# Kernel tuning notes

Measured on AMD Instinct MI355X. Metric: run time of the kernel, lower is better.

Reference implementation:

```python
import jax, jax.numpy as jnp
import numpy as np

B, S, E, H, K = 64, 512, 256, 512, 100


def setup_inputs() -> dict:
    key = jax.random.key(0)
    ks = jax.random.split(key, 7)
    scale = 0.02
    return {
        "event_types": jax.random.randint(ks[0], (B, S), 0, K),
        "time_deltas": jax.random.uniform(ks[1], (B, S), dtype=jnp.float32),
        "embedding": jax.random.normal(ks[2], (K, E), dtype=jnp.float32) * scale,
        "W": jax.random.normal(ks[3], (E + H, 5 * H), dtype=jnp.float32) * scale,
        "b": jnp.zeros((5 * H,), dtype=jnp.float32),
        "Wi": jax.random.normal(ks[4], (H, K), dtype=jnp.float32) * scale,
        "bi": jnp.zeros((K,), dtype=jnp.float32),
    }


def _ctlstm_scan(x_seq, dt_seq, W, b, hidden_dim):
    """x_seq: [B,S,E], dt_seq: [B,S]. Returns h_seq [B,S,H], decay_seq [B,S,H]."""
    bsz = x_seq.shape[0]
    h0 = jnp.zeros((bsz, hidden_dim), x_seq.dtype)
    c0 = jnp.zeros((bsz, hidden_dim), x_seq.dtype)

    def step(carry, inp):
        h, c = carry
        x_t, dt_t = inp  # [B,E], [B]
        z = jnp.concatenate([x_t, h], axis=-1) @ W + b  # [B,5H]
        i, f, o, g, d = jnp.split(z, 5, axis=-1)
        i = jax.nn.sigmoid(i)
        f = jax.nn.sigmoid(f)
        o = jax.nn.sigmoid(o)
        g = jnp.tanh(g)
        decay = jax.nn.softplus(d)  # decay rate >= 0
        c_new = f * c + i * g
        c_t = c_new * jnp.exp(-decay * dt_t[:, None])  # continuous-time decay
        h_t = o * jnp.tanh(c_t)
        return (h_t, c_t), (h_t, decay)

    # time-major for scan
    xs = (jnp.swapaxes(x_seq, 0, 1), jnp.swapaxes(dt_seq, 0, 1))
    _, (h_seq, decay_seq) = jax.lax.scan(step, (h0, c0), xs)
    return jnp.swapaxes(h_seq, 0, 1), jnp.swapaxes(decay_seq, 0, 1)


def reference(event_types, time_deltas, embedding, W, b, Wi, bi):
    x_seq = embedding[event_types]  # [B,S,E]
    hidden_state, decay_rate = _ctlstm_scan(x_seq, time_deltas, W, b, H)
    base_intensities = jax.nn.softplus(hidden_state @ Wi + bi)  # [B,S,K]
    return hidden_state, decay_rate, base_intensities
```

## Files before the change

### kernel.cpp

```cpp
#include <hip/hip_runtime.h>
#include <hip/hip_bf16.h>
#include <stdint.h>

#define BB 64
#define SS 512
#define EE 256
#define HH 512
#define NWG 32

typedef short s16x8 __attribute__((ext_vector_type(8)));
typedef float vf4 __attribute__((ext_vector_type(4)));

#define OFF_WBT   0UL
#define OFF_EMB   3932160UL
#define OFF_WIT   3983360UL
#define OFF_DTT   4098048UL
#define OFF_FLAGS 4229120UL
#define OFF_HBUF  4491264UL
#define OFF_ZXP   38045696UL

__device__ __forceinline__ int fidx(int t, int w, int v) {
  return (((t >> 4) * 128) + w * 4 + v) * 16 + (t & 15);
}

__device__ __forceinline__ unsigned short f2bf(float f) {
  unsigned u = __float_as_uint(f);
  u += 0x7fffu + ((u >> 16) & 1u);
  return (unsigned short)(u >> 16);
}
__device__ __forceinline__ float bf2f(unsigned short h) {
  return __uint_as_float(((unsigned)h) << 16);
}
__device__ __forceinline__ float sigmoidf_(float x) { return 1.f / (1.f + __expf(-x)); }
__device__ __forceinline__ float softplusf_(float x) {
  return fmaxf(x, 0.f) + log1pf(__expf(-fabsf(x)));
}
__device__ __forceinline__ float tanhf_(float x) {
  float e = __expf(2.f * x);
  return 1.f - 2.f / (e + 1.f);
}

__global__ void init_kernel(const float* __restrict__ W, const float* __restrict__ emb,
                            const float* __restrict__ Wi, const float* __restrict__ td,
                            unsigned short* __restrict__ WbT, unsigned short* __restrict__ embB,
                            unsigned short* __restrict__ WiT, float* __restrict__ dtT,
                            int* __restrict__ flags) {
  unsigned i = blockIdx.x * 256u + threadIdx.x;
  if (i < 1966080u) {
    unsigned c = i / 768u, k = i % 768u;
    WbT[i] = f2bf(W[(size_t)k * 2560u + c]);
    return;
  }
  i -= 1966080u;
  if (i < 25600u) { embB[i] = f2bf(emb[i]); return; }
  i -= 25600u;
  if (i < 57344u) {
    unsigned c = i / 512u, k = i % 512u;
    WiT[i] = f2bf(c < 100u ? Wi[(size_t)k * 100u + c] : 0.f);
    return;
  }
  i -= 57344u;
  if (i < 32768u) {
    unsigned t = i / 64u, b = i % 64u;
    dtT[i] = td[(size_t)b * 512u + t];
    return;
  }
  i -= 32768u;
  if (i < 65536u) { flags[i] = 0; return; }
}

__global__ __launch_bounds__(256, 2)
void zx_kernel(const int* __restrict__ evt, const unsigned short* __restrict__ embB,
               const unsigned short* __restrict__ WbT, const float* __restrict__ bias,
               unsigned short* __restrict__ zxp) {
  const int t = blockIdx.y;
  const int tid = threadIdx.x;
  const int v = tid >> 6, lane = tid & 63;
  const int m = lane & 15, quad = lane >> 4;
  const int cbase = blockIdx.x * 256 + v * 64;

  s16x8 Breg[8][4];
#pragma unroll
  for (int cf = 0; cf < 4; ++cf) {
    const unsigned short* bp = WbT + (size_t)(cbase + cf * 16 + m) * 768 + quad * 8;
#pragma unroll
    for (int ch = 0; ch < 8; ++ch) Breg[ch][cf] = *(const s16x8*)(bp + ch * 32);
  }
  int ev[4];
#pragma unroll
  for (int rt = 0; rt < 4; ++rt) ev[rt] = evt[(size_t)(rt * 16 + m) * 512 + t];

  vf4 acc[4][4];
#pragma unroll
  for (int cf = 0; cf < 4; ++cf) {
    float bbv = bias[cbase + cf * 16 + m];
#pragma unroll
    for (int rt = 0; rt < 4; ++rt) acc[rt][cf] = (vf4){bbv, bbv, bbv, bbv};
  }
#pragma unroll
  for (int ch = 0; ch < 8; ++ch) {
#pragma unroll
    for (int rt = 0; rt < 4; ++rt) {
      s16x8 a = *(const s16x8*)(embB + (size_t)ev[rt] * 256 + ch * 32 + quad * 8);
#pragma unroll
      for (int cf = 0; cf < 4; ++cf)
        acc[rt][cf] = __builtin_amdgcn_mfma_f32_16x16x32_bf16(a, Breg[ch][cf], acc[rt][cf], 0, 0, 0);
    }
  }
#pragma unroll
  for (int cf = 0; cf < 4; ++cf) {
    int col0 = cbase + cf * 16;
    int g = col0 >> 9;
    int w = (col0 & 511) >> 4;
#pragma unroll
    for (int rt = 0; rt < 4; ++rt) {
      unsigned h0 = f2bf(acc[rt][cf][0]);
      unsigned h1 = f2bf(acc[rt][cf][1]);
      unsigned h2 = f2bf(acc[rt][cf][2]);
      unsigned h3 = f2bf(acc[rt][cf][3]);
      uint2 val;
      val.x = h0 | (h1 << 16);
      val.y = h2 | (h3 << 16);
      ((uint2*)zxp)[((((size_t)t * 32 + w) * 4 + rt) * 5 + g) * 64 + lane] = val;
    }
  }
}

__global__ __launch_bounds__(256, 1)
void scan_kernel(const unsigned short* __restrict__ WbT,
                 const unsigned short* __restrict__ zxp,
                 const float* __restrict__ dtT,
                 unsigned short* __restrict__ hbuf,
                 int* __restrict__ flags,
                 float* __restrict__ out_h, float* __restrict__ out_d) {
  const int w = blockIdx.x;
  const int tid = threadIdx.x;
  const int v = tid >> 6, lane = tid & 63;
  const int m = lane & 15, quad = lane >> 4;
  const int rowb = v * 16;
  const int bb0 = rowb + quad * 4;
  const int col = w * 16 + m;

  s16x8 Breg[16][5];
#pragma unroll
  for (int g = 0; g < 5; ++g) {
    const unsigned short* bp = WbT + (size_t)(g * 512 + w * 16 + m) * 768 + 256 + quad * 8;
#pragma unroll
    for (int ch = 0; ch < 16; ++ch) Breg[ch][g] = *(const s16x8*)(bp + ch * 32);
  }

  vf4 cst = (vf4){0.f, 0.f, 0.f, 0.f};

  for (int t = 0; t < 512; ++t) {
    vf4 acc[5];
#pragma unroll
    for (int g = 0; g < 5; ++g) {
      uint2 zv = ((const uint2*)zxp)[((((size_t)t * 32 + w) * 4 + v) * 5 + g) * 64 + lane];
      acc[g][0] = bf2f((unsigned short)(zv.x & 0xffffu));
      acc[g][1] = bf2f((unsigned short)(zv.x >> 16));
      acc[g][2] = bf2f((unsigned short)(zv.y & 0xffffu));
      acc[g][3] = bf2f((unsigned short)(zv.y >> 16));
    }
    vf4 dt4 = *(const vf4*)(dtT + t * 64 + bb0);

    if (t > 0) {
      const int tp = t - 1;
      if (lane < 32) {
        const int* fp = flags + fidx(tp, lane, v);
        while (__hip_atomic_load(fp, __ATOMIC_RELAXED, __HIP_MEMORY_SCOPE_AGENT) == 0) {
          __builtin_amdgcn_s_sleep(1);
        }
      }
      __asm__ __volatile__("" ::: "memory");
      const unsigned short* hsrc =
          hbuf + (size_t)tp * (BB * HH) + (size_t)(rowb + m) * HH + quad * 8;
#pragma unroll
      for (int ch = 0; ch < 16; ++ch) {
        s16x8 a = *(const s16x8*)(hsrc + ch * 32);
#pragma unroll
        for (int g = 0; g < 5; ++g)
          acc[g] = __builtin_amdgcn_mfma_f32_16x16x32_bf16(a, Breg[ch][g], acc[g], 0, 0, 0);
      }
    }

    float hv[4], dv[4];
#pragma unroll
    for (int r = 0; r < 4; ++r) {
      float i_ = sigmoidf_(acc[0][r]);
      float f_ = sigmoidf_(acc[1][r]);
      float o_ = sigmoidf_(acc[2][r]);
      float g_ = tanhf_(acc[3][r]);
      float dec = softplusf_(acc[4][r]);
      float cn = f_ * cst[r] + i_ * g_;
      float ct = cn * __expf(-dec * dt4[r]);
      float h_ = o_ * tanhf_(ct);
      cst[r] = ct;
      hv[r] = h_; dv[r] = dec;
      __hip_atomic_store(hbuf + (size_t)t * (BB * HH) + (size_t)(bb0 + r) * HH + col,
                         f2bf(h_), __ATOMIC_RELAXED, __HIP_MEMORY_SCOPE_AGENT);
    }
    __asm__ __volatile__("" ::: "memory");
    __builtin_amdgcn_s_waitcnt(0);
    __asm__ __volatile__("" ::: "memory");
    if (lane == 0) {
      __hip_atomic_store(flags + fidx(t, w, v), 1, __ATOMIC_RELAXED,
                         __HIP_MEMORY_SCOPE_AGENT);
    }
#pragma unroll
    for (int r = 0; r < 4; ++r) {
      size_t oo = ((size_t)(bb0 + r) * SS + t) * HH + col;
      out_h[oo] = hv[r];
      out_d[oo] = dv[r];
    }
  }
}

__global__ __launch_bounds__(256, 2)
void inten_kernel(const unsigned short* __restrict__ hbuf,
                  const unsigned short* __restrict__ WiT,
                  const float* __restrict__ bi,
                  float* __restrict__ out_i) {
  const int b = blockIdx.y;
  const int t0 = blockIdx.x * 64;
  const int tid = threadIdx.x;
  const int v = tid >> 6, lane = tid & 63;
  const int m = lane & 15, quad = lane >> 4;
  const int trow = t0 + v * 16 + m;

  vf4 acc[7];
#pragma unroll
  for (int cf = 0; cf < 7; ++cf) {
    int c = cf * 16 + m;
    float bbv = (c < 100) ? bi[c] : 0.f;
    acc[cf] = (vf4){bbv, bbv, bbv, bbv};
  }
  const unsigned short* ha = hbuf + ((size_t)trow * 64 + b) * 512 + quad * 8;
#pragma unroll 4
  for (int ch = 0; ch < 16; ++ch) {
    s16x8 a = *(const s16x8*)(ha + ch * 32);
#pragma unroll
    for (int cf = 0; cf < 7; ++cf) {
      s16x8 bf = *(const s16x8*)(WiT + (size_t)(cf * 16 + m) * 512 + ch * 32 + quad * 8);
      acc[cf] = __builtin_amdgcn_mfma_f32_16x16x32_bf16(a, bf, acc[cf], 0, 0, 0);
    }
  }
#pragma unroll
  for (int cf = 0; cf < 7; ++cf) {
    int c = cf * 16 + m;
#pragma unroll
    for (int r = 0; r < 4; ++r) {
      int tt = t0 + v * 16 + quad * 4 + r;
      if (c < 100) out_i[((size_t)b * 512 + tt) * 100 + c] = softplusf_(acc[cf][r]);
    }
  }
}

extern "C" void kernel_launch(void* const* d_in, const int* in_sizes, int n_in,
                              void* d_out, int out_size, void* d_ws, size_t ws_size,
                              hipStream_t stream) {
  (void)in_sizes; (void)n_in; (void)out_size; (void)ws_size;
  const int*   evt  = (const int*)d_in[0];
  const float* td   = (const float*)d_in[1];
  const float* emb  = (const float*)d_in[2];
  const float* W    = (const float*)d_in[3];
  const float* bias = (const float*)d_in[4];
  const float* Wi   = (const float*)d_in[5];
  const float* bi   = (const float*)d_in[6];

  char* ws = (char*)d_ws;
  unsigned short* WbT  = (unsigned short*)(ws + OFF_WBT);
  unsigned short* embB = (unsigned short*)(ws + OFF_EMB);
  unsigned short* WiT  = (unsigned short*)(ws + OFF_WIT);
  float*          dtT  = (float*)(ws + OFF_DTT);
  int*            flags= (int*)(ws + OFF_FLAGS);
  unsigned short* hbuf = (unsigned short*)(ws + OFF_HBUF);
  unsigned short* zxp  = (unsigned short*)(ws + OFF_ZXP);

  float* out_h = (float*)d_out;
  float* out_d = out_h + (size_t)BB * SS * HH;
  float* out_i = out_d + (size_t)BB * SS * HH;

  init_kernel<<<8390, 256, 0, stream>>>(W, emb, Wi, td, WbT, embB, WiT, dtT, flags);
  zx_kernel<<<dim3(10, 512), 256, 0, stream>>>(evt, embB, WbT, bias, zxp);
  scan_kernel<<<NWG, 256, 0, stream>>>(WbT, zxp, dtT, hbuf, flags, out_h, out_d);
  inten_kernel<<<dim3(8, 64), 256, 0, stream>>>(hbuf, WiT, bi, out_i);
}
```

Before: 3.703 ms.

## Split scan into batch groups with XCC-local sync and independent recurrences

The recurrent scan now runs on 64 workgroups instead of 32. It is split into 8 independent batch groups of 8 rows, and each group spreads the hidden columns over 8 workgroups, so a group only waits on its own 8 producers rather than on every workgroup. The h buffer and the zx layout are reorganised per batch group. At startup the kernel reads which XCC each workgroup landed on; if a group sits entirely on one XCC it uses workgroup-scope atomics and volatile stores for lower-latency flag polling. The cost is that half of each MFMA's 16 rows are padding, and the flag and XCC co-location handshake adds complexity and risk.

Result: slower. 4.878 ms (+31.7%).

```diff
diff --git a/kernel.cpp b/kernel.cpp
--- a/kernel.cpp
+++ b/kernel.cpp
@@ -6,7 +6,6 @@
 #define SS 512
 #define EE 256
 #define HH 512
-#define NWG 32
 
 typedef short s16x8 __attribute__((ext_vector_type(8)));
 typedef float vf4 __attribute__((ext_vector_type(4)));
@@ -16,11 +15,12 @@
 #define OFF_WIT   3983360UL
 #define OFF_DTT   4098048UL
 #define OFF_FLAGS 4229120UL
-#define OFF_HBUF  4491264UL
-#define OFF_ZXP   38045696UL
-
-__device__ __forceinline__ int fidx(int t, int w, int v) {
-  return (((t >> 4) * 128) + w * 4 + v) * 16 + (t & 15);
+#define OFF_CTL   4753408UL
+#define OFF_HB    4753920UL
+#define OFF_ZXP   38308352UL
+
+__device__ __forceinline__ int fidx(int t, int g, int L) {
+  return (((t >> 4) * 256) + g * 32 + L) * 16 + (t & 15);
 }
 
 __device__ __forceinline__ unsigned short f2bf(float f) {
@@ -66,7 +66,7 @@
     return;
   }
   i -= 32768u;
-  if (i < 65536u) { flags[i] = 0; return; }
+  if (i < 131200u) { flags[i] = 0; return; }
 }
 
 __global__ __launch_bounds__(256, 2)
@@ -110,10 +110,13 @@
 #pragma unroll
   for (int cf = 0; cf < 4; ++cf) {
     int col0 = cbase + cf * 16;
-    int g = col0 >> 9;
-    int w = (col0 & 511) >> 4;
+    int gate = col0 >> 9;
+    int hcol = col0 & 511;
+    int rr_ = hcol >> 6;
+    int vv = (hcol >> 4) & 3;
 #pragma unroll
     for (int rt = 0; rt < 4; ++rt) {
+      int gg = rt * 2 + (quad >> 1);
       unsigned h0 = f2bf(acc[rt][cf][0]);
       unsigned h1 = f2bf(acc[rt][cf][1]);
       unsigned h2 = f2bf(acc[rt][cf][2]);
@@ -121,7 +124,8 @@
       uint2 val;
       val.x = h0 | (h1 << 16);
       val.y = h2 | (h3 << 16);
-      ((uint2*)zxp)[((((size_t)t * 32 + w) * 4 + rt) * 5 + g) * 64 + lane] = val;
+      ((uint2*)zxp)[(((((size_t)t * 8 + gg) * 8 + rr_) * 4 + vv) * 5 + gate) * 32
+                    + (quad & 1) * 16 + m] = val;
     }
   }
 }
@@ -130,93 +134,127 @@
 void scan_kernel(const unsigned short* __restrict__ WbT,
                  const unsigned short* __restrict__ zxp,
                  const float* __restrict__ dtT,
-                 unsigned short* __restrict__ hbuf,
-                 int* __restrict__ flags,
+                 unsigned short* __restrict__ hb,
+                 int* __restrict__ flags, int* __restrict__ ctl,
                  float* __restrict__ out_h, float* __restrict__ out_d) {
-  const int w = blockIdx.x;
+  const int wg = blockIdx.x;
+  const int g = wg & 7, r = wg >> 3;
   const int tid = threadIdx.x;
   const int v = tid >> 6, lane = tid & 63;
   const int m = lane & 15, quad = lane >> 4;
-  const int rowb = v * 16;
-  const int bb0 = rowb + quad * 4;
-  const int col = w * 16 + m;
+  const int qh = quad & 1;
+  const int c0 = r * 64 + v * 16;
+  const int col = c0 + m;
+
+  __shared__ int s_loc;
+  if (tid == 0) {
+    unsigned xcc = __builtin_amdgcn_s_getreg(63508) & 0xfu;
+    __hip_atomic_store(&ctl[wg], (int)(xcc + 1u), __ATOMIC_RELAXED, __HIP_MEMORY_SCOPE_AGENT);
+    __hip_atomic_fetch_add(&ctl[64], 1, __ATOMIC_RELEASE, __HIP_MEMORY_SCOPE_AGENT);
+    while (__hip_atomic_load(&ctl[64], __ATOMIC_ACQUIRE, __HIP_MEMORY_SCOPE_AGENT) < 64)
+      __builtin_amdgcn_s_sleep(1);
+    int x0 = __hip_atomic_load(&ctl[g], __ATOMIC_RELAXED, __HIP_MEMORY_SCOPE_AGENT);
+    int lc = (x0 != 0);
+    for (int j = 1; j < 8; ++j)
+      lc &= (__hip_atomic_load(&ctl[g + 8 * j], __ATOMIC_RELAXED, __HIP_MEMORY_SCOPE_AGENT) == x0);
+    s_loc = lc;
+  }
+  __syncthreads();
+  const bool loc = (s_loc != 0);
 
   s16x8 Breg[16][5];
 #pragma unroll
-  for (int g = 0; g < 5; ++g) {
-    const unsigned short* bp = WbT + (size_t)(g * 512 + w * 16 + m) * 768 + 256 + quad * 8;
-#pragma unroll
-    for (int ch = 0; ch < 16; ++ch) Breg[ch][g] = *(const s16x8*)(bp + ch * 32);
+  for (int g5 = 0; g5 < 5; ++g5) {
+    const unsigned short* bp = WbT + (size_t)(g5 * 512 + c0 + m) * 768 + 256 + quad * 8;
+#pragma unroll
+    for (int ch = 0; ch < 16; ++ch) Breg[ch][g5] = *(const s16x8*)(bp + ch * 32);
   }
 
   vf4 cst = (vf4){0.f, 0.f, 0.f, 0.f};
 
   for (int t = 0; t < 512; ++t) {
     vf4 acc[5];
-#pragma unroll
-    for (int g = 0; g < 5; ++g) {
-      uint2 zv = ((const uint2*)zxp)[((((size_t)t * 32 + w) * 4 + v) * 5 + g) * 64 + lane];
-      acc[g][0] = bf2f((unsigned short)(zv.x & 0xffffu));
-      acc[g][1] = bf2f((unsigned short)(zv.x >> 16));
-      acc[g][2] = bf2f((unsigned short)(zv.y & 0xffffu));
-      acc[g][3] = bf2f((unsigned short)(zv.y >> 16));
-    }
-    vf4 dt4 = *(const vf4*)(dtT + t * 64 + bb0);
+    if (lane < 32) {
+#pragma unroll
+      for (int g5 = 0; g5 < 5; ++g5) {
+        uint2 zv = ((const uint2*)zxp)[(((((size_t)t * 8 + g) * 8 + r) * 4 + v) * 5 + g5) * 32 + lane];
+        acc[g5][0] = bf2f((unsigned short)(zv.x & 0xffffu));
+        acc[g5][1] = bf2f((unsigned short)(zv.x >> 16));
+        acc[g5][2] = bf2f((unsigned short)(zv.y & 0xffffu));
+        acc[g5][3] = bf2f((unsigned short)(zv.y >> 16));
+      }
+    } else {
+#pragma unroll
+      for (int g5 = 0; g5 < 5; ++g5) acc[g5] = (vf4){0.f, 0.f, 0.f, 0.f};
+    }
+    vf4 dt4 = *(const vf4*)(dtT + t * 64 + g * 8 + qh * 4);
 
     if (t > 0) {
       const int tp = t - 1;
       if (lane < 32) {
-        const int* fp = flags + fidx(tp, lane, v);
-        while (__hip_atomic_load(fp, __ATOMIC_RELAXED, __HIP_MEMORY_SCOPE_AGENT) == 0) {
-          __builtin_amdgcn_s_sleep(1);
+        int* fp = flags + fidx(tp, g, lane);
+        if (loc) {
+          while ((__hip_atomic_fetch_add(fp, 0x10000, __ATOMIC_RELAXED,
+                                         __HIP_MEMORY_SCOPE_WORKGROUP) & 0xffff) == 0) {}
+        } else {
+          while (__hip_atomic_load(fp, __ATOMIC_RELAXED, __HIP_MEMORY_SCOPE_AGENT) == 0)
+            __builtin_amdgcn_s_sleep(1);
         }
       }
       __asm__ __volatile__("" ::: "memory");
-      const unsigned short* hsrc =
-          hbuf + (size_t)tp * (BB * HH) + (size_t)(rowb + m) * HH + quad * 8;
+      const unsigned short* hsrc = hb + (((size_t)g * 512 + tp) * 8 + (m & 7)) * 512 + quad * 8;
 #pragma unroll
       for (int ch = 0; ch < 16; ++ch) {
         s16x8 a = *(const s16x8*)(hsrc + ch * 32);
 #pragma unroll
-        for (int g = 0; g < 5; ++g)
-          acc[g] = __builtin_amdgcn_mfma_f32_16x16x32_bf16(a, Breg[ch][g], acc[g], 0, 0, 0);
+        for (int g5 = 0; g5 < 5; ++g5)
+          acc[g5] = __builtin_amdgcn_mfma_f32_16x16x32_bf16(a, Breg[ch][g5], acc[g5], 0, 0, 0);
       }
     }
 
     float hv[4], dv[4];
 #pragma unroll
-    for (int r = 0; r < 4; ++r) {
-      float i_ = sigmoidf_(acc[0][r]);
-      float f_ = sigmoidf_(acc[1][r]);
-      float o_ = sigmoidf_(acc[2][r]);
-      float g_ = tanhf_(acc[3][r]);
-      float dec = softplusf_(acc[4][r]);
-      float cn = f_ * cst[r] + i_ * g_;
-      float ct = cn * __expf(-dec * dt4[r]);
+    for (int rr = 0; rr < 4; ++rr) {
+      float i_ = sigmoidf_(acc[0][rr]);
+      float f_ = sigmoidf_(acc[1][rr]);
+      float o_ = sigmoidf_(acc[2][rr]);
+      float g_ = tanhf_(acc[3][rr]);
+      float dec = softplusf_(acc[4][rr]);
+      float cn = f_ * cst[rr] + i_ * g_;
+      float ct = cn * __expf(-dec * dt4[rr]);
       float h_ = o_ * tanhf_(ct);
-      cst[r] = ct;
-      hv[r] = h_; dv[r] = dec;
-      __hip_atomic_store(hbuf + (size_t)t * (BB * HH) + (size_t)(bb0 + r) * HH + col,
-                         f2bf(h_), __ATOMIC_RELAXED, __HIP_MEMORY_SCOPE_AGENT);
+      cst[rr] = ct;
+      hv[rr] = h_; dv[rr] = dec;
+    }
+    if (quad < 2) {
+#pragma unroll
+      for (int rr = 0; rr < 4; ++rr) {
+        unsigned short* hp = hb + (((size_t)g * 512 + t) * 8 + quad * 4 + rr) * 512 + col;
+        if (loc) *(volatile unsigned short*)hp = f2bf(hv[rr]);
+        else __hip_atomic_store(hp, f2bf(hv[rr]), __ATOMIC_RELAXED, __HIP_MEMORY_SCOPE_AGENT);
+      }
     }
     __asm__ __volatile__("" ::: "memory");
-    __builtin_amdgcn_s_waitcnt(0);
-    __asm__ __volatile__("" ::: "memory");
+    asm volatile("s_waitcnt vmcnt(0)" ::: "memory");
     if (lane == 0) {
-      __hip_atomic_store(flags + fidx(t, w, v), 1, __ATOMIC_RELAXED,
-                         __HIP_MEMORY_SCOPE_AGENT);
-    }
-#pragma unroll
-    for (int r = 0; r < 4; ++r) {
-      size_t oo = ((size_t)(bb0 + r) * SS + t) * HH + col;
-      out_h[oo] = hv[r];
-      out_d[oo] = dv[r];
+      int* fp = flags + fidx(t, g, r * 4 + v);
+      if (loc) (void)__hip_atomic_exchange(fp, 1, __ATOMIC_RELAXED, __HIP_MEMORY_SCOPE_WORKGROUP);
+      else __hip_atomic_store(fp, 1, __ATOMIC_RELAXED, __HIP_MEMORY_SCOPE_AGENT);
+    }
+    if (quad < 2) {
+#pragma unroll
+      for (int rr = 0; rr < 4; ++rr) {
+        int b_ = g * 8 + quad * 4 + rr;
+        size_t oo = ((size_t)b_ * SS + t) * HH + col;
+        out_h[oo] = hv[rr];
+        out_d[oo] = dv[rr];
+      }
     }
   }
 }
 
 __global__ __launch_bounds__(256, 2)
-void inten_kernel(const unsigned short* __restrict__ hbuf,
+void inten_kernel(const unsigned short* __restrict__ hb,
                   const unsigned short* __restrict__ WiT,
                   const float* __restrict__ bi,
                   float* __restrict__ out_i) {
@@ -234,7 +272,7 @@
     float bbv = (c < 100) ? bi[c] : 0.f;
     acc[cf] = (vf4){bbv, bbv, bbv, bbv};
   }
-  const unsigned short* ha = hbuf + ((size_t)trow * 64 + b) * 512 + quad * 8;
+  const unsigned short* ha = hb + (((size_t)(b >> 3) * 512 + trow) * 8 + (b & 7)) * 512 + quad * 8;
 #pragma unroll 4
   for (int ch = 0; ch < 16; ++ch) {
     s16x8 a = *(const s16x8*)(ha + ch * 32);
@@ -248,9 +286,9 @@
   for (int cf = 0; cf < 7; ++cf) {
     int c = cf * 16 + m;
 #pragma unroll
-    for (int r = 0; r < 4; ++r) {
-      int tt = t0 + v * 16 + quad * 4 + r;
-      if (c < 100) out_i[((size_t)b * 512 + tt) * 100 + c] = softplusf_(acc[cf][r]);
+    for (int rr = 0; rr < 4; ++rr) {
+      int tt = t0 + v * 16 + quad * 4 + rr;
+      if (c < 100) out_i[((size_t)b * 512 + tt) * 100 + c] = softplusf_(acc[cf][rr]);
     }
   }
 }
@@ -273,15 +311,16 @@
   unsigned short* WiT  = (unsigned short*)(ws + OFF_WIT);
   float*          dtT  = (float*)(ws + OFF_DTT);
   int*            flags= (int*)(ws + OFF_FLAGS);
-  unsigned short* hbuf = (unsigned short*)(ws + OFF_HBUF);
+  int*            ctl  = (int*)(ws + OFF_CTL);
+  unsigned short* hb   = (unsigned short*)(ws + OFF_HB);
   unsigned short* zxp  = (unsigned short*)(ws + OFF_ZXP);
 
   float* out_h = (float*)d_out;
   float* out_d = out_h + (size_t)BB * SS * HH;
   float* out_i = out_d + (size_t)BB * SS * HH;
 
-  init_kernel<<<8390, 256, 0, stream>>>(W, emb, Wi, td, WbT, embB, WiT, dtT, flags);
+  init_kernel<<<8645, 256, 0, stream>>>(W, emb, Wi, td, WbT, embB, WiT, dtT, flags);
   zx_kernel<<<dim3(10, 512), 256, 0, stream>>>(evt, embB, WbT, bias, zxp);
-  scan_kernel<<<NWG, 256, 0, stream>>>(WbT, zxp, dtT, hbuf, flags, out_h, out_d);
-  inten_kernel<<<dim3(8, 64), 256, 0, stream>>>(hbuf, WiT, bi, out_i);
-}
+  scan_kernel<<<64, 256, 0, stream>>>(WbT, zxp, dtT, hb, flags, ctl, out_h, out_d);
+  inten_kernel<<<dim3(8, 64), 256, 0, stream>>>(hb, WiT, bi, out_i);
+}
```
